# Performance work log

Measured on AMD Instinct MI355X. Metric: run time of the kernel, lower is better.

## Reference

```python
import jax, jax.numpy as jnp
import numpy as np

B, T, N, H = 256, 128, 512, 512
LB, UB = 0.0, 0.1
MAX_IT = 32  # bounded substitute for the data-dependent while loop (converges in a few iters)


def setup_inputs() -> dict:
    key = jax.random.key(0)
    ks = jax.random.split(key, 11)
    s = 1.0 / np.sqrt(H)
    u = lambda k, shape: jax.random.uniform(k, shape, jnp.float32, -s, s)
    return {
        "x": jax.random.normal(ks[0], (B, T, N), jnp.float32),
        "W_ih0": u(ks[1], (3 * H, N)), "W_hh0": u(ks[2], (3 * H, H)),
        "b_ih0": u(ks[3], (3 * H,)), "b_hh0": u(ks[4], (3 * H,)),
        "W_ih1": u(ks[5], (3 * H, H)), "W_hh1": u(ks[6], (3 * H, H)),
        "b_ih1": u(ks[7], (3 * H,)), "b_hh1": u(ks[8], (3 * H,)),
        "fc_w": u(ks[9], (N, H)), "fc_b": u(ks[10], (N,)),
    }


def gru_layer(x, W_ih, W_hh, b_ih, b_hh):
    # x: [B, T, I] -> hidden sequence [B, T, H]; matches torch.nn.GRU gate math.
    xi = jnp.einsum('bti,gi->btg', x, W_ih) + b_ih  # precompute input proj [B,T,3H]

    def step(h, xi_t):
        gh = h @ W_hh.T + b_hh
        xr, xz, xn = jnp.split(xi_t, 3, axis=-1)
        hr, hz, hn = jnp.split(gh, 3, axis=-1)
        r = jax.nn.sigmoid(xr + hr)
        z = jax.nn.sigmoid(xz + hz)
        n = jnp.tanh(xn + r * hn)
        h2 = (1.0 - z) * n + z * h
        return h2, h2

    h0 = jnp.zeros((x.shape[0], H), x.dtype)
    _, hs = jax.lax.scan(step, h0, jnp.swapaxes(xi, 0, 1))
    return jnp.swapaxes(hs, 0, 1)


def rebalance(w):
    # Water-filling: clamp to [LB, UB], redistribute clipped mass to non-capped
    # names proportionally, repeat until no weight exceeds UB. Bounded iteration
    # count with masked no-op updates (do-while semantics: body runs at least once).
    wc0 = jnp.clip(w, LB, UB)

    def body(st, _):
        old, wc, cont = st
        leftover = jnp.sum(old - wc)
        mask = wc != UB
        noms = jnp.where(mask, wc, 0.0)
        gift = leftover * noms / jnp.sum(noms)
        wc2 = wc + gift                      # gift is 0 where mask is False
        again = jnp.any(wc2 > UB)
        wc_next = jnp.where(again, jnp.clip(wc2, LB, UB), wc2)
        old_n = jnp.where(cont, wc2, old)
        wc_n = jnp.where(cont, wc_next, wc)
        return (old_n, wc_n, jnp.logical_and(cont, again)), None

    (old, wc, _), _ = jax.lax.scan(body, (w, wc0, jnp.array(True)), None, length=MAX_IT)
    return wc


def reference(x, W_ih0, W_hh0, b_ih0, b_hh0, W_ih1, W_hh1, b_ih1, b_hh1, fc_w, fc_b):
    h = gru_layer(x, W_ih0, W_hh0, b_ih0, b_hh0)
    h = gru_layer(h, W_ih1, W_hh1, b_ih1, b_hh1)
    h_t = h[:, -1, :]                        # last timestep [B, H]
    logit = h_t @ fc_w.T + fc_b              # dropout is identity in eval
    logit = jax.nn.softmax(jax.nn.silu(logit), axis=-1)
    return jax.vmap(rebalance)(logit)
```

## Files before the change

### kernel.cpp

```cpp
#include <hip/hip_runtime.h>
#include <math.h>

#define BB 256
#define TT 128
#define NN 512
#define HH 512
#define G3 1536
#define SLAB (HH * BB)
#define XSLAB (G3 * BB)
#define CH 16

typedef __attribute__((ext_vector_type(8))) short bf16x8;
typedef __attribute__((ext_vector_type(4))) float f32x4;
typedef unsigned short ushort;

__device__ __forceinline__ ushort bf16_rne(float f) {
    union { float f; unsigned u; } v; v.f = f;
    unsigned r = (v.u + 0x7fffu + ((v.u >> 16) & 1u)) >> 16;
    return (ushort)r;
}
__device__ __forceinline__ float bf16_tof(ushort h) {
    union { float f; unsigned u; } v; v.u = ((unsigned)h) << 16;
    return v.f;
}
__device__ __forceinline__ float sigm(float v) { return 1.f / (1.f + expf(-v)); }

__global__ __launch_bounds__(256) void zero6(
    float* h0s, float* h1s, ushort* H0hs, ushort* H0ls, ushort* H1hs, ushort* H1ls) {
    int i = blockIdx.x * 256 + threadIdx.x;
    int sel = i / 65536, r = i % 65536;
    if (sel == 0)      ((float2*)h0s)[r] = {0.f, 0.f};
    else if (sel == 1) ((float2*)h1s)[r] = {0.f, 0.f};
    else if (sel == 2) { if (r < 32768) ((uint2*)H0hs)[r] = {0u, 0u}; }
    else if (sel == 3) { if (r < 32768) ((uint2*)H0ls)[r] = {0u, 0u}; }
    else if (sel == 4) { if (r < 32768) ((uint2*)H1hs)[r] = {0u, 0u}; }
    else               { if (r < 32768) ((uint2*)H1ls)[r] = {0u, 0u}; }
}

__global__ __launch_bounds__(256) void convert_split(
    const float* __restrict__ in, ushort* __restrict__ hi,
    ushort* __restrict__ lo, int n) {
    int i = (blockIdx.x * 256 + threadIdx.x) * 4;
    if (i >= n) return;
    float4 v = *(const float4*)(in + i);
    float f[4] = {v.x, v.y, v.z, v.w};
    ushort h[4], l[4];
#pragma unroll
    for (int q = 0; q < 4; ++q) {
        ushort hh = bf16_rne(f[q]);
        h[q] = hh;
        l[q] = bf16_rne(f[q] - bf16_tof(hh));
    }
    *(ushort4*)(hi + i) = *(ushort4*)h;
    *(ushort4*)(lo + i) = *(ushort4*)l;
}

__global__ __launch_bounds__(64) void pack_swz(
    const float* __restrict__ Whh0, const float* __restrict__ Wih1,
    const float* __restrict__ Whh1, ushort* __restrict__ pk) {
    const int bi = blockIdx.x;
    const int it = bi & 3, kq = (bi >> 2) & 3, p = (bi >> 4) & 31, sec = bi >> 9;
    const float* W = (sec == 0) ? Whh0 : (sec == 1) ? Wih1 : Whh1;
    const int lane = threadIdx.x;
    const int l15 = lane & 15, l4 = lane >> 4;
    ushort* base = pk + (size_t)bi * 3072 + lane * 8;
#pragma unroll
    for (int g = 0; g < 3; ++g) {
        int grow = g * 512 + p * 16 + l15;
        const float* src = W + (size_t)grow * 512 + kq * 128 + it * 32 + l4 * 8;
        ushort hs[8], ls[8];
#pragma unroll
        for (int e = 0; e < 8; ++e) {
            float v = src[e];
            ushort h = bf16_rne(v);
            hs[e] = h;
            ls[e] = bf16_rne(v - bf16_tof(h));
        }
        *(uint4*)(base + g * 1024) = *(uint4*)hs;
        *(uint4*)(base + g * 1024 + 512) = *(uint4*)ls;
    }
}

__global__ __launch_bounds__(256) void xi_mfma_x(
    const ushort* __restrict__ Wh, const ushort* __restrict__ Wl,
    const float* __restrict__ x, int t0,
    const float* __restrict__ bias, float* __restrict__ out) {
    __shared__ ushort As[2][128][40];
    __shared__ ushort Bs[2][128][40];
    const int tid = threadIdx.x;
    const int n0 = blockIdx.x * 128;
    const int g0 = blockIdx.y * 128;
    const int tl = n0 >> 8, b0 = n0 & 255;
    const int tg = t0 + tl;
    const int w = tid >> 6, lane = tid & 63;
    const int wg = (w >> 1) * 64, wb = (w & 1) * 64;
    const int l15 = lane & 15, l4 = lane >> 4;
    const int sr = tid >> 2, sc = (tid & 3) * 8;

    f32x4 acc[4][4] = {};
    for (int kc = 0; kc < 512; kc += 32) {
        uint4 a0 = *(const uint4*)(Wh + (size_t)(g0 + sr) * 512 + kc + sc);
        uint4 a1 = *(const uint4*)(Wh + (size_t)(g0 + 64 + sr) * 512 + kc + sc);
        uint4 a2 = *(const uint4*)(Wl + (size_t)(g0 + sr) * 512 + kc + sc);
        uint4 a3 = *(const uint4*)(Wl + (size_t)(g0 + 64 + sr) * 512 + kc + sc);
        const float* xr0 = x + ((size_t)(b0 + sr) * TT + tg) * NN + kc + sc;
        const float* xr1 = x + ((size_t)(b0 + 64 + sr) * TT + tg) * NN + kc + sc;
        float4 f00 = *(const float4*)xr0, f01 = *(const float4*)(xr0 + 4);
        float4 f10 = *(const float4*)xr1, f11 = *(const float4*)(xr1 + 4);
        float fa[8] = {f00.x, f00.y, f00.z, f00.w, f01.x, f01.y, f01.z, f01.w};
        float fb[8] = {f10.x, f10.y, f10.z, f10.w, f11.x, f11.y, f11.z, f11.w};
        ushort h0v[8], l0v[8], h1v[8], l1v[8];
#pragma unroll
        for (int q = 0; q < 8; ++q) {
            ushort hh = bf16_rne(fa[q]);
            h0v[q] = hh; l0v[q] = bf16_rne(fa[q] - bf16_tof(hh));
            hh = bf16_rne(fb[q]);
            h1v[q] = hh; l1v[q] = bf16_rne(fb[q] - bf16_tof(hh));
        }
        __syncthreads();
        *(uint4*)&As[0][sr][sc] = a0;      *(uint4*)&As[0][64 + sr][sc] = a1;
        *(uint4*)&As[1][sr][sc] = a2;      *(uint4*)&As[1][64 + sr][sc] = a3;
        *(uint4*)&Bs[0][sr][sc] = *(uint4*)h0v;  *(uint4*)&Bs[0][64 + sr][sc] = *(uint4*)h1v;
        *(uint4*)&Bs[1][sr][sc] = *(uint4*)l0v;  *(uint4*)&Bs[1][64 + sr][sc] = *(uint4*)l1v;
        __syncthreads();
        bf16x8 ah[4], al[4], bh[4], bl[4];
#pragma unroll
        for (int i = 0; i < 4; ++i) {
            ah[i] = *(const bf16x8*)&As[0][wg + 16 * i + l15][l4 * 8];
            al[i] = *(const bf16x8*)&As[1][wg + 16 * i + l15][l4 * 8];
            bh[i] = *(const bf16x8*)&Bs[0][wb + 16 * i + l15][l4 * 8];
            bl[i] = *(const bf16x8*)&Bs[1][wb + 16 * i + l15][l4 * 8];
        }
#pragma unroll
        for (int i = 0; i < 4; ++i)
#pragma unroll
            for (int j = 0; j < 4; ++j) {
                acc[i][j] = __builtin_amdgcn_mfma_f32_16x16x32_bf16(ah[i], bh[j], acc[i][j], 0, 0, 0);
                acc[i][j] = __builtin_amdgcn_mfma_f32_16x16x32_bf16(ah[i], bl[j], acc[i][j], 0, 0, 0);
                acc[i][j] = __builtin_amdgcn_mfma_f32_16x16x32_bf16(al[i], bh[j], acc[i][j], 0, 0, 0);
            }
    }
    float* op = out + (size_t)tl * XSLAB;
#pragma unroll
    for (int i = 0; i < 4; ++i) {
        int gbase = g0 + wg + 16 * i + l4 * 4;
#pragma unroll
        for (int r = 0; r < 4; ++r) {
            float bv = bias[gbase + r];
#pragma unroll
            for (int j = 0; j < 4; ++j)
                op[(size_t)(gbase + r) * 256 + b0 + wb + 16 * j + l15] = acc[i][j][r] + bv;
        }
    }
}

template <int NG>
__device__ __forceinline__ void kreduceN(float* scr, int kq, int ct, int l15, int l4,
                                         f32x4* acc) {
    const int SS = NG * 272;
    const int slot = (kq >> 1) * 2 + ct;
    const int pos0 = (l4 * 4) * 17 + l15;
    __syncthreads();
    if (kq & 1) {
#pragma unroll
        for (int g = 0; g < NG; ++g)
#pragma unroll
            for (int q = 0; q < 4; ++q)
                scr[slot * SS + g * 272 + pos0 + q * 17] = acc[g][q];
    }
    __syncthreads();
    if (!(kq & 1)) {
#pragma unroll
        for (int g = 0; g < NG; ++g)
#pragma unroll
            for (int q = 0; q < 4; ++q)
                acc[g][q] += scr[slot * SS + g * 272 + pos0 + q * 17];
    }
    if (kq == 2) {
#pragma unroll
        for (int g = 0; g < NG; ++g)
#pragma unroll
            for (int q = 0; q < 4; ++q)
                scr[(2 + ct) * SS + g * 272 + pos0 + q * 17] = acc[g][q];
    }
    __syncthreads();
    if (kq == 0) {
#pragma unroll
        for (int g = 0; g < NG; ++g)
#pragma unroll
            for (int q = 0; q < 4; ++q)
                acc[g][q] += scr[(2 + ct) * SS + g * 272 + pos0 + q * 17];
    }
}

__global__ __launch_bounds__(512) void step_v11(
    int s, const ushort* __restrict__ pk,
    const float* __restrict__ xi0,
    const float* __restrict__ bih1,
    const float* __restrict__ bhh0, const float* __restrict__ bhh1,
    float* __restrict__ h0f, float* __restrict__ h1f,
    ushort* __restrict__ H0h, ushort* __restrict__ H0l,
    ushort* __restrict__ H1h, ushort* __restrict__ H1l) {
    __shared__ float scr[6528];
    const int bi = blockIdx.x;
    const int sec = bi >> 8, local = bi & 255;
    const int t = (sec == 0) ? s : s - 1;
    if (t < 0 || t > 127) return;
    const int p = (local & 7) * 4 + ((local >> 3) & 3);
    const int b0 = (local >> 5) * 32;
    const int tid = threadIdx.x, w = tid >> 6, lane = tid & 63;
    const int l15 = lane & 15, l4 = lane >> 4;
    const int kq = w >> 1, ct = w & 1;
    const int brow = b0 + ct * 16 + l15;

    if (sec == 0) {
        const int sl = (t - 1) & 1;
        const ushort* Bh = H0h + (size_t)sl * SLAB;
        const ushort* Bl = H0l + (size_t)sl * SLAB;
        const ushort* baseA = pk + (size_t)((0 * 32 + p) * 4 + kq) * 12288 + lane * 8;
        const ushort* bhp = Bh + (size_t)brow * 512 + kq * 128 + l4 * 8;
        const ushort* blp = Bl + (size_t)brow * 512 + kq * 128 + l4 * 8;
        f32x4 acc[3] = {};
#pragma unroll
        for (int it = 0; it < 4; ++it) {
            bf16x8 bh = *(const bf16x8*)(bhp + it * 32);
            bf16x8 bl = *(const bf16x8*)(blp + it * 32);
#pragma unroll
            for (int g = 0; g < 3; ++g) {
                const ushort* rec = baseA + (it * 3 + g) * 1024;
                bf16x8 ah = *(const bf16x8*)rec;
                bf16x8 al = *(const bf16x8*)(rec + 512);
                acc[g] = __builtin_amdgcn_mfma_f32_16x16x32_bf16(ah, bh, acc[g], 0, 0, 0);
                acc[g] = __builtin_amdgcn_mfma_f32_16x16x32_bf16(ah, bl, acc[g], 0, 0, 0);
                acc[g] = __builtin_amdgcn_mfma_f32_16x16x32_bf16(al, bh, acc[g], 0, 0, 0);
            }
        }
        kreduceN<3>(scr, kq, ct, l15, l4, acc);
        if (kq == 0) {
            const float* xi = xi0 + (size_t)(t & (CH - 1)) * XSLAB;
            const float* hpv = h0f + (size_t)((t - 1) & 1) * SLAB;
            float* hnew = h0f + (size_t)(t & 1) * SLAB;
            ushort* Hh = H0h + (size_t)(t & 1) * SLAB;
            ushort* Hl = H0l + (size_t)(t & 1) * SLAB;
            const int b = brow;
            ushort hq[4], lq[4];
#pragma unroll
            for (int q = 0; q < 4; ++q) {
                int jrow = p * 16 + l4 * 4 + q;
                float xr = xi[(size_t)jrow * 256 + b];
                float xz = xi[(size_t)(512 + jrow) * 256 + b];
                float xn = xi[(size_t)(1024 + jrow) * 256 + b];
                float hp = hpv[(size_t)jrow * 256 + b];
                float rr = sigm(xr + acc[0][q] + bhh0[jrow]);
                float zz = sigm(xz + acc[1][q] + bhh0[512 + jrow]);
                float nn = tanhf(xn + rr * (acc[2][q] + bhh0[1024 + jrow]));
                float hv = (1.f - zz) * nn + zz * hp;
                hnew[(size_t)jrow * 256 + b] = hv;
                ushort hh = bf16_rne(hv);
                hq[q] = hh;
                lq[q] = bf16_rne(hv - bf16_tof(hh));
            }
            size_t o = (size_t)b * 512 + p * 16 + l4 * 4;
            *(ushort4*)(Hh + o) = *(ushort4*)hq;
            *(ushort4*)(Hl + o) = *(ushort4*)lq;
        }
    } else {
        const int slX = t & 1, slG = (t - 1) & 1;
        const ushort* BhX = H0h + (size_t)slX * SLAB;
        const ushort* BlX = H0l + (size_t)slX * SLAB;
        const ushort* BhG = H1h + (size_t)slG * SLAB;
        const ushort* BlG = H1l + (size_t)slG * SLAB;
        const ushort* baseAX = pk + (size_t)((1 * 32 + p) * 4 + kq) * 12288 + lane * 8;
        const ushort* baseAG = pk + (size_t)((2 * 32 + p) * 4 + kq) * 12288 + lane * 8;
        const ushort* bhpX = BhX + (size_t)brow * 512 + kq * 128 + l4 * 8;
        const ushort* blpX = BlX + (size_t)brow * 512 + kq * 128 + l4 * 8;
        const ushort* bhpG = BhG + (size_t)brow * 512 + kq * 128 + l4 * 8;
        const ushort* blpG = BlG + (size_t)brow * 512 + kq * 128 + l4 * 8;
        f32x4 acc[6] = {};
#pragma unroll
        for (int it = 0; it < 4; ++it) {
            bf16x8 bhX = *(const bf16x8*)(bhpX + it * 32);
            bf16x8 blX = *(const bf16x8*)(blpX + it * 32);
            bf16x8 bhG = *(const bf16x8*)(bhpG + it * 32);
            bf16x8 blG = *(const bf16x8*)(blpG + it * 32);
#pragma unroll
            for (int g = 0; g < 3; ++g) {
                const ushort* recX = baseAX + (it * 3 + g) * 1024;
                const ushort* recG = baseAG + (it * 3 + g) * 1024;
                bf16x8 ahX = *(const bf16x8*)recX;
                bf16x8 alX = *(const bf16x8*)(recX + 512);
                bf16x8 ahG = *(const bf16x8*)recG;
                bf16x8 alG = *(const bf16x8*)(recG + 512);
                acc[g] = __builtin_amdgcn_mfma_f32_16x16x32_bf16(ahX, bhX, acc[g], 0, 0, 0);
                acc[g] = __builtin_amdgcn_mfma_f32_16x16x32_bf16(ahX, blX, acc[g], 0, 0, 0);
                acc[g] = __builtin_amdgcn_mfma_f32_16x16x32_bf16(alX, bhX, acc[g], 0, 0, 0);
                acc[3 + g] = __builtin_amdgcn_mfma_f32_16x16x32_bf16(ahG, bhG, acc[3 + g], 0, 0, 0);
                acc[3 + g] = __builtin_amdgcn_mfma_f32_16x16x32_bf16(ahG, blG, acc[3 + g], 0, 0, 0);
                acc[3 + g] = __builtin_amdgcn_mfma_f32_16x16x32_bf16(alG, bhG, acc[3 + g], 0, 0, 0);
            }
        }
        kreduceN<6>(scr, kq, ct, l15, l4, acc);
        if (kq == 0) {
            const float* hpv = h1f + (size_t)((t - 1) & 1) * SLAB;
            float* hnew = h1f + (size_t)(t & 1) * SLAB;
            ushort* Hh = H1h + (size_t)(t & 1) * SLAB;
            ushort* Hl = H1l + (size_t)(t & 1) * SLAB;
            const int b = brow;
            ushort hq[4], lq[4];
#pragma unroll
            for (int q = 0; q < 4; ++q) {
                int jrow = p * 16 + l4 * 4 + q;
                float xr = acc[0][q] + bih1[jrow];
                float xz = acc[1][q] + bih1[512 + jrow];
                float xn = acc[2][q] + bih1[1024 + jrow];
                float hp = hpv[(size_t)jrow * 256 + b];
                float rr = sigm(xr + acc[3][q] + bhh1[jrow]);
                float zz = sigm(xz + acc[4][q] + bhh1[512 + jrow]);
                float nn = tanhf(xn + rr * (acc[5][q] + bhh1[1024 + jrow]));
                float hv = (1.f - zz) * nn + zz * hp;
                hnew[(size_t)jrow * 256 + b] = hv;
                ushort hh = bf16_rne(hv);
                hq[q] = hh;
                lq[q] = bf16_rne(hv - bf16_tof(hh));
            }
            size_t o = (size_t)b * 512 + p * 16 + l4 * 4;
            *(ushort4*)(Hh + o) = *(ushort4*)hq;
            *(ushort4*)(Hl + o) = *(ushort4*)lq;
        }
    }
}


__global__ __launch_bounds__(256) void hT_to_h(
    const float* __restrict__ hT, float* __restrict__ h) {
    __shared__ float tb[64][65];
    const int tid = threadIdx.x;
    const int k0 = blockIdx.x * 64, b0 = blockIdx.y * 64;
#pragma unroll
    for (int i = 0; i < 4; ++i) {
        int r = (tid >> 4) + 16 * i, c = (tid & 15) * 4;
        float4 v = *(const float4*)(hT + (size_t)(k0 + r) * 256 + b0 + c);
        tb[c + 0][r] = v.x; tb[c + 1][r] = v.y; tb[c + 2][r] = v.z; tb[c + 3][r] = v.w;
    }
    __syncthreads();
#pragma unroll
    for (int i = 0; i < 4; ++i) {
        int r = (tid >> 4) + 16 * i, c = (tid & 15) * 4;
        float4 v;
        v.x = tb[r][c]; v.y = tb[r][c + 1]; v.z = tb[r][c + 2]; v.w = tb[r][c + 3];
        *(float4*)(h + (size_t)(b0 + r) * 512 + k0 + c) = v;
    }
}

__device__ __forceinline__ float blockReduceSum(float v, float* tmp) {
    __syncthreads();
#pragma unroll
    for (int o = 32; o; o >>= 1) v += __shfl_down(v, o);
    if ((threadIdx.x & 63) == 0) tmp[threadIdx.x >> 6] = v;
    __syncthreads();
    if (threadIdx.x == 0) tmp[4] = tmp[0] + tmp[1] + tmp[2] + tmp[3];
    __syncthreads();
    return tmp[4];
}

__device__ __forceinline__ float blockReduceMax(float v, float* tmp) {
    __syncthreads();
#pragma unroll
    for (int o = 32; o; o >>= 1) v = fmaxf(v, __shfl_down(v, o));
    if ((threadIdx.x & 63) == 0) tmp[threadIdx.x >> 6] = v;
    __syncthreads();
    if (threadIdx.x == 0) tmp[4] = fmaxf(fmaxf(tmp[0], tmp[1]), fmaxf(tmp[2], tmp[3]));
    __syncthreads();
    return tmp[4];
}

__global__ __launch_bounds__(256) void head_kernel(
    const float* __restrict__ h1, const float* __restrict__ fcw,
    const float* __restrict__ fcb, float* __restrict__ out) {
    __shared__ __align__(16) float hrow[512];
    __shared__ float wv[512];
    __shared__ float ov[512];
    __shared__ float tmp[8];
    const int b = blockIdx.x, tid = threadIdx.x;
    hrow[tid]       = h1[(size_t)b * 512 + tid];
    hrow[tid + 256] = h1[(size_t)b * 512 + 256 + tid];
    __syncthreads();

    float s[2];
#pragma unroll
    for (int q = 0; q < 2; ++q) {
        int n = tid + q * 256;
        const float* wr = fcw + (size_t)n * 512;
        float acc = 0.f;
        for (int k = 0; k < 512; k += 4) {
            float4 wq = *(const float4*)(wr + k);
            acc += wq.x * hrow[k] + wq.y * hrow[k + 1] + wq.z * hrow[k + 2] + wq.w * hrow[k + 3];
        }
        float l = acc + fcb[n];
        s[q] = l / (1.f + expf(-l));
    }

    float mx = blockReduceMax(fmaxf(s[0], s[1]), tmp);
    float e0 = expf(s[0] - mx), e1 = expf(s[1] - mx);
    float sum = blockReduceSum(e0 + e1, tmp);
    float w0 = e0 / sum, w1 = e1 / sum;

    ov[tid] = w0;       ov[tid + 256] = w1;
    wv[tid]       = fminf(fmaxf(w0, 0.f), 0.1f);
    wv[tid + 256] = fminf(fmaxf(w1, 0.f), 0.1f);
    __syncthreads();

    for (int it = 0; it < 32; ++it) {
        float wc0 = wv[tid], wc1 = wv[tid + 256];
        float o0 = ov[tid], o1 = ov[tid + 256];
        float leftover = blockReduceSum((o0 - wc0) + (o1 - wc1), tmp);
        float n0 = (wc0 != 0.1f) ? wc0 : 0.f;
        float n1 = (wc1 != 0.1f) ? wc1 : 0.f;
        float denom = blockReduceSum(n0 + n1, tmp);
        float w20 = wc0 + leftover * n0 / denom;
        float w21 = wc1 + leftover * n1 / denom;
        float fl = ((w20 > 0.1f) || (w21 > 0.1f)) ? 1.f : 0.f;
        bool again = blockReduceSum(fl, tmp) > 0.f;
        __syncthreads();
        ov[tid] = w20; ov[tid + 256] = w21;
        wv[tid]       = again ? fminf(fmaxf(w20, 0.f), 0.1f) : w20;
        wv[tid + 256] = again ? fminf(fmaxf(w21, 0.f), 0.1f) : w21;
        __syncthreads();
        if (!again) break;
    }

    out[(size_t)b * 512 + tid]       = wv[tid];
    out[(size_t)b * 512 + 256 + tid] = wv[tid + 256];
}

extern "C" void kernel_launch(void* const* d_in, const int* in_sizes, int n_in,
                              void* d_out, int out_size, void* d_ws, size_t ws_size,
                              hipStream_t stream) {
    const float* x    = (const float*)d_in[0];
    const float* Wih0 = (const float*)d_in[1];
    const float* Whh0 = (const float*)d_in[2];
    const float* bih0 = (const float*)d_in[3];
    const float* bhh0 = (const float*)d_in[4];
    const float* Wih1 = (const float*)d_in[5];
    const float* Whh1 = (const float*)d_in[6];
    const float* bih1 = (const float*)d_in[7];
    const float* bhh1 = (const float*)d_in[8];
    const float* fcw  = (const float*)d_in[9];
    const float* fcb  = (const float*)d_in[10];
    float* out = (float*)d_out;

    const size_t WHALF = (size_t)G3 * HH;
    ushort* W0h = (ushort*)d_ws;
    ushort* W0l = W0h + WHALF;
    ushort* pk  = W0l + WHALF;
    float* xi0 = (float*)(pk + (size_t)1536 * 3072);
    float* h0f = xi0 + (size_t)CH * XSLAB;
    float* h1f = h0f + 2 * (size_t)SLAB;
    float* h1n = h1f + 2 * (size_t)SLAB;
    ushort* H0h = (ushort*)(h1n + SLAB);
    ushort* H0l = H0h + 2 * (size_t)SLAB;
    ushort* H1h = H0l + 2 * (size_t)SLAB;
    ushort* H1l = H1h + 2 * (size_t)SLAB;

    convert_split<<<(G3 * HH) / 1024, 256, 0, stream>>>(Wih0, W0h, W0l, G3 * HH);
    pack_swz<<<1536, 64, 0, stream>>>(Whh0, Wih1, Whh1, pk);
    zero6<<<1536, 256, 0, stream>>>(h0f + SLAB, h1f + SLAB,
                                    H0h + SLAB, H0l + SLAB, H1h + SLAB, H1l + SLAB);

    for (int c = 0; c < TT / CH; ++c) {
        xi_mfma_x<<<dim3(CH * 2, 12), 256, 0, stream>>>(W0h, W0l, x, c * CH, bih0, xi0);
        for (int tl = 0; tl < CH; ++tl) {
            int s = c * CH + tl;
            step_v11<<<512, 512, 0, stream>>>(s, pk, xi0, bih1, bhh0, bhh1,
                                              h0f, h1f, H0h, H0l, H1h, H1l);
        }
    }
    step_v11<<<512, 512, 0, stream>>>(128, pk, xi0, bih1, bhh0, bhh1,
                                      h0f, h1f, H0h, H0l, H1h, H1l);

    hT_to_h<<<dim3(8, 4), 256, 0, stream>>>(h1f + SLAB, h1n);
    head_kernel<<<BB, 256, 0, stream>>>(h1n, fcw, fcb, out);
}
```

Before: 2.196 ms.

## Fuse input projection into recurrent step kernel and drop fp32 hidden state

The layer-0 input projection now runs as a third section of the per-timestep step kernel, computing timestep s+8 alongside the recurrence, so the separate chunked xi launches go away and that work overlaps the latency-bound recurrent steps. The fp32 hidden-state buffers are removed; the previous hidden value is rebuilt from its bf16 hi/lo split, which saves global writes and removes the transpose kernel before the head. The costs are 768 blocks per step instead of 512, extra register and LDS pressure, a ring-buffer dependency on the 8-step lookahead fitting in the 16-slot xi buffer, and a slight precision loss from reconstructing h out of two bf16 halves.

New measurement: 2.653 ms. +20.8%, slower.

```diff
diff --git a/kernel.cpp b/kernel.cpp
--- a/kernel.cpp
+++ b/kernel.cpp
@@ -25,16 +25,26 @@
 }
 __device__ __forceinline__ float sigm(float v) { return 1.f / (1.f + expf(-v)); }
 
-__global__ __launch_bounds__(256) void zero6(
-    float* h0s, float* h1s, ushort* H0hs, ushort* H0ls, ushort* H1hs, ushort* H1ls) {
+__device__ __forceinline__ void split8(float4 a, float4 b, uint4& hi, uint4& lo) {
+    float f[8] = {a.x, a.y, a.z, a.w, b.x, b.y, b.z, b.w};
+    ushort hs[8], ls[8];
+#pragma unroll
+    for (int q = 0; q < 8; ++q) {
+        ushort h = bf16_rne(f[q]);
+        hs[q] = h;
+        ls[q] = bf16_rne(f[q] - bf16_tof(h));
+    }
+    hi = *(uint4*)hs;
+    lo = *(uint4*)ls;
+}
+
+__global__ __launch_bounds__(256) void zero4(
+    ushort* a, ushort* b, ushort* c, ushort* d) {
     int i = blockIdx.x * 256 + threadIdx.x;
-    int sel = i / 65536, r = i % 65536;
-    if (sel == 0)      ((float2*)h0s)[r] = {0.f, 0.f};
-    else if (sel == 1) ((float2*)h1s)[r] = {0.f, 0.f};
-    else if (sel == 2) { if (r < 32768) ((uint2*)H0hs)[r] = {0u, 0u}; }
-    else if (sel == 3) { if (r < 32768) ((uint2*)H0ls)[r] = {0u, 0u}; }
-    else if (sel == 4) { if (r < 32768) ((uint2*)H1hs)[r] = {0u, 0u}; }
-    else               { if (r < 32768) ((uint2*)H1ls)[r] = {0u, 0u}; }
+    int sel = i >> 14, r = i & 16383;
+    uint4 z = {0u, 0u, 0u, 0u};
+    ushort* p = (sel == 0) ? a : (sel == 1) ? b : (sel == 2) ? c : d;
+    ((uint4*)p)[r] = z;
 }
 
 __global__ __launch_bounds__(256) void convert_split(
@@ -107,21 +117,14 @@
         const float* xr1 = x + ((size_t)(b0 + 64 + sr) * TT + tg) * NN + kc + sc;
         float4 f00 = *(const float4*)xr0, f01 = *(const float4*)(xr0 + 4);
         float4 f10 = *(const float4*)xr1, f11 = *(const float4*)(xr1 + 4);
-        float fa[8] = {f00.x, f00.y, f00.z, f00.w, f01.x, f01.y, f01.z, f01.w};
-        float fb[8] = {f10.x, f10.y, f10.z, f10.w, f11.x, f11.y, f11.z, f11.w};
-        ushort h0v[8], l0v[8], h1v[8], l1v[8];
-#pragma unroll
-        for (int q = 0; q < 8; ++q) {
-            ushort hh = bf16_rne(fa[q]);
-            h0v[q] = hh; l0v[q] = bf16_rne(fa[q] - bf16_tof(hh));
-            hh = bf16_rne(fb[q]);
-            h1v[q] = hh; l1v[q] = bf16_rne(fb[q] - bf16_tof(hh));
-        }
+        uint4 h0v, l0v, h1v, l1v;
+        split8(f00, f01, h0v, l0v);
+        split8(f10, f11, h1v, l1v);
         __syncthreads();
         *(uint4*)&As[0][sr][sc] = a0;      *(uint4*)&As[0][64 + sr][sc] = a1;
         *(uint4*)&As[1][sr][sc] = a2;      *(uint4*)&As[1][64 + sr][sc] = a3;
-        *(uint4*)&Bs[0][sr][sc] = *(uint4*)h0v;  *(uint4*)&Bs[0][64 + sr][sc] = *(uint4*)h1v;
-        *(uint4*)&Bs[1][sr][sc] = *(uint4*)l0v;  *(uint4*)&Bs[1][64 + sr][sc] = *(uint4*)l1v;
+        *(uint4*)&Bs[0][sr][sc] = h0v;     *(uint4*)&Bs[0][64 + sr][sc] = h1v;
+        *(uint4*)&Bs[1][sr][sc] = l0v;     *(uint4*)&Bs[1][64 + sr][sc] = l1v;
         __syncthreads();
         bf16x8 ah[4], al[4], bh[4], bl[4];
 #pragma unroll
@@ -193,19 +196,18 @@
     }
 }
 
-__global__ __launch_bounds__(512) void step_v11(
+__global__ __launch_bounds__(512) void step_v12(
     int s, const ushort* __restrict__ pk,
-    const float* __restrict__ xi0,
-    const float* __restrict__ bih1,
+    const float* __restrict__ x,
+    const ushort* __restrict__ W0h, const ushort* __restrict__ W0l,
+    float* __restrict__ xi0,
+    const float* __restrict__ bih0, const float* __restrict__ bih1,
     const float* __restrict__ bhh0, const float* __restrict__ bhh1,
-    float* __restrict__ h0f, float* __restrict__ h1f,
     ushort* __restrict__ H0h, ushort* __restrict__ H0l,
     ushort* __restrict__ H1h, ushort* __restrict__ H1l) {
     __shared__ float scr[6528];
     const int bi = blockIdx.x;
     const int sec = bi >> 8, local = bi & 255;
-    const int t = (sec == 0) ? s : s - 1;
-    if (t < 0 || t > 127) return;
     const int p = (local & 7) * 4 + ((local >> 3) & 3);
     const int b0 = (local >> 5) * 32;
     const int tid = threadIdx.x, w = tid >> 6, lane = tid & 63;
@@ -214,6 +216,8 @@
     const int brow = b0 + ct * 16 + l15;
 
     if (sec == 0) {
+        const int t = s;
+        if (t > 127) return;
         const int sl = (t - 1) & 1;
         const ushort* Bh = H0h + (size_t)sl * SLAB;
         const ushort* Bl = H0l + (size_t)sl * SLAB;
@@ -238,11 +242,16 @@
         kreduceN<3>(scr, kq, ct, l15, l4, acc);
         if (kq == 0) {
             const float* xi = xi0 + (size_t)(t & (CH - 1)) * XSLAB;
-            const float* hpv = h0f + (size_t)((t - 1) & 1) * SLAB;
-            float* hnew = h0f + (size_t)(t & 1) * SLAB;
+            const ushort* Hph = H0h + (size_t)sl * SLAB;
+            const ushort* Hpl = H0l + (size_t)sl * SLAB;
             ushort* Hh = H0h + (size_t)(t & 1) * SLAB;
             ushort* Hl = H0l + (size_t)(t & 1) * SLAB;
             const int b = brow;
+            size_t o = (size_t)b * 512 + p * 16 + l4 * 4;
+            ushort4 hph = *(const ushort4*)(Hph + o);
+            ushort4 hpl = *(const ushort4*)(Hpl + o);
+            const ushort* hph_ = (const ushort*)&hph;
+            const ushort* hpl_ = (const ushort*)&hpl;
             ushort hq[4], lq[4];
 #pragma unroll
             for (int q = 0; q < 4; ++q) {
@@ -250,21 +259,21 @@
                 float xr = xi[(size_t)jrow * 256 + b];
                 float xz = xi[(size_t)(512 + jrow) * 256 + b];
                 float xn = xi[(size_t)(1024 + jrow) * 256 + b];
-                float hp = hpv[(size_t)jrow * 256 + b];
+                float hp = bf16_tof(hph_[q]) + bf16_tof(hpl_[q]);
                 float rr = sigm(xr + acc[0][q] + bhh0[jrow]);
                 float zz = sigm(xz + acc[1][q] + bhh0[512 + jrow]);
                 float nn = tanhf(xn + rr * (acc[2][q] + bhh0[1024 + jrow]));
                 float hv = (1.f - zz) * nn + zz * hp;
-                hnew[(size_t)jrow * 256 + b] = hv;
                 ushort hh = bf16_rne(hv);
                 hq[q] = hh;
                 lq[q] = bf16_rne(hv - bf16_tof(hh));
             }
-            size_t o = (size_t)b * 512 + p * 16 + l4 * 4;
             *(ushort4*)(Hh + o) = *(ushort4*)hq;
             *(ushort4*)(Hl + o) = *(ushort4*)lq;
         }
-    } else {
+    } else if (sec == 1) {
+        const int t = s - 1;
+        if (t < 0 || t > 127) return;
         const int slX = t & 1, slG = (t - 1) & 1;
         const ushort* BhX = H0h + (size_t)slX * SLAB;
         const ushort* BlX = H0l + (size_t)slX * SLAB;
@@ -301,11 +310,17 @@
         }
         kreduceN<6>(scr, kq, ct, l15, l4, acc);
         if (kq == 0) {
-            const float* hpv = h1f + (size_t)((t - 1) & 1) * SLAB;
-            float* hnew = h1f + (size_t)(t & 1) * SLAB;
+            const int slp = (t - 1) & 1;
+            const ushort* Hph = H1h + (size_t)slp * SLAB;
+            const ushort* Hpl = H1l + (size_t)slp * SLAB;
             ushort* Hh = H1h + (size_t)(t & 1) * SLAB;
             ushort* Hl = H1l + (size_t)(t & 1) * SLAB;
             const int b = brow;
+            size_t o = (size_t)b * 512 + p * 16 + l4 * 4;
+            ushort4 hph = *(const ushort4*)(Hph + o);
+            ushort4 hpl = *(const ushort4*)(Hpl + o);
+            const ushort* hph_ = (const ushort*)&hph;
+            const ushort* hpl_ = (const ushort*)&hpl;
             ushort hq[4], lq[4];
 #pragma unroll
             for (int q = 0; q < 4; ++q) {
@@ -313,44 +328,56 @@
                 float xr = acc[0][q] + bih1[jrow];
                 float xz = acc[1][q] + bih1[512 + jrow];
                 float xn = acc[2][q] + bih1[1024 + jrow];
-                float hp = hpv[(size_t)jrow * 256 + b];
+                float hp = bf16_tof(hph_[q]) + bf16_tof(hpl_[q]);
                 float rr = sigm(xr + acc[3][q] + bhh1[jrow]);
                 float zz = sigm(xz + acc[4][q] + bhh1[512 + jrow]);
                 float nn = tanhf(xn + rr * (acc[5][q] + bhh1[1024 + jrow]));
                 float hv = (1.f - zz) * nn + zz * hp;
-                hnew[(size_t)jrow * 256 + b] = hv;
                 ushort hh = bf16_rne(hv);
                 hq[q] = hh;
                 lq[q] = bf16_rne(hv - bf16_tof(hh));
             }
-            size_t o = (size_t)b * 512 + p * 16 + l4 * 4;
             *(ushort4*)(Hh + o) = *(ushort4*)hq;
             *(ushort4*)(Hl + o) = *(ushort4*)lq;
         }
-    }
-}
-
-
-__global__ __launch_bounds__(256) void hT_to_h(
-    const float* __restrict__ hT, float* __restrict__ h) {
-    __shared__ float tb[64][65];
-    const int tid = threadIdx.x;
-    const int k0 = blockIdx.x * 64, b0 = blockIdx.y * 64;
-#pragma unroll
-    for (int i = 0; i < 4; ++i) {
-        int r = (tid >> 4) + 16 * i, c = (tid & 15) * 4;
-        float4 v = *(const float4*)(hT + (size_t)(k0 + r) * 256 + b0 + c);
-        tb[c + 0][r] = v.x; tb[c + 1][r] = v.y; tb[c + 2][r] = v.z; tb[c + 3][r] = v.w;
-    }
-    __syncthreads();
-#pragma unroll
-    for (int i = 0; i < 4; ++i) {
-        int r = (tid >> 4) + 16 * i, c = (tid & 15) * 4;
-        float4 v;
-        v.x = tb[r][c]; v.y = tb[r][c + 1]; v.z = tb[r][c + 2]; v.w = tb[r][c + 3];
-        *(float4*)(h + (size_t)(b0 + r) * 512 + k0 + c) = v;
-    }
-}
+    } else {
+        const int tt = s + 8;
+        if (tt > 127) return;
+        const float* xb = x + ((size_t)brow * TT + tt) * NN;
+        f32x4 acc[3] = {};
+#pragma unroll
+        for (int it = 0; it < 4; ++it) {
+            const int k = kq * 128 + it * 32 + l4 * 8;
+            float4 f0 = *(const float4*)(xb + k);
+            float4 f1 = *(const float4*)(xb + k + 4);
+            uint4 bhv, blv;
+            split8(f0, f1, bhv, blv);
+            bf16x8 bh = *(bf16x8*)&bhv, bl = *(bf16x8*)&blv;
+#pragma unroll
+            for (int g = 0; g < 3; ++g) {
+                int grow = g * 512 + p * 16 + l15;
+                bf16x8 ah = *(const bf16x8*)(W0h + (size_t)grow * 512 + k);
+                bf16x8 al = *(const bf16x8*)(W0l + (size_t)grow * 512 + k);
+                acc[g] = __builtin_amdgcn_mfma_f32_16x16x32_bf16(ah, bh, acc[g], 0, 0, 0);
+                acc[g] = __builtin_amdgcn_mfma_f32_16x16x32_bf16(ah, bl, acc[g], 0, 0, 0);
+                acc[g] = __builtin_amdgcn_mfma_f32_16x16x32_bf16(al, bh, acc[g], 0, 0, 0);
+            }
+        }
+        kreduceN<3>(scr, kq, ct, l15, l4, acc);
+        if (kq == 0) {
+            float* xo = xi0 + (size_t)(tt & (CH - 1)) * XSLAB;
+            const int b = brow;
+#pragma unroll
+            for (int g = 0; g < 3; ++g)
+#pragma unroll
+                for (int q = 0; q < 4; ++q) {
+                    int grow = g * 512 + p * 16 + l4 * 4 + q;
+                    xo[(size_t)grow * 256 + b] = acc[g][q] + bih0[grow];
+                }
+        }
+    }
+}
+
 
 __device__ __forceinline__ float blockReduceSum(float v, float* tmp) {
     __syncthreads();
@@ -375,15 +402,19 @@
 }
 
 __global__ __launch_bounds__(256) void head_kernel(
-    const float* __restrict__ h1, const float* __restrict__ fcw,
-    const float* __restrict__ fcb, float* __restrict__ out) {
+    const ushort* __restrict__ H1hs, const ushort* __restrict__ H1ls,
+    const float* __restrict__ fcw, const float* __restrict__ fcb,
+    float* __restrict__ out) {
     __shared__ __align__(16) float hrow[512];
     __shared__ float wv[512];
     __shared__ float ov[512];
     __shared__ float tmp[8];
     const int b = blockIdx.x, tid = threadIdx.x;
-    hrow[tid]       = h1[(size_t)b * 512 + tid];
-    hrow[tid + 256] = h1[(size_t)b * 512 + 256 + tid];
+    {
+        size_t o = (size_t)b * 512 + tid;
+        hrow[tid]       = bf16_tof(H1hs[o]) + bf16_tof(H1ls[o]);
+        hrow[tid + 256] = bf16_tof(H1hs[o + 256]) + bf16_tof(H1ls[o + 256]);
+    }
     __syncthreads();
 
     float s[2];
@@ -454,30 +485,20 @@
     ushort* W0l = W0h + WHALF;
     ushort* pk  = W0l + WHALF;
     float* xi0 = (float*)(pk + (size_t)1536 * 3072);
-    float* h0f = xi0 + (size_t)CH * XSLAB;
-    float* h1f = h0f + 2 * (size_t)SLAB;
-    float* h1n = h1f + 2 * (size_t)SLAB;
-    ushort* H0h = (ushort*)(h1n + SLAB);
+    ushort* H0h = (ushort*)(xi0 + (size_t)CH * XSLAB);
     ushort* H0l = H0h + 2 * (size_t)SLAB;
     ushort* H1h = H0l + 2 * (size_t)SLAB;
     ushort* H1l = H1h + 2 * (size_t)SLAB;
 
     convert_split<<<(G3 * HH) / 1024, 256, 0, stream>>>(Wih0, W0h, W0l, G3 * HH);
     pack_swz<<<1536, 64, 0, stream>>>(Whh0, Wih1, Whh1, pk);
-    zero6<<<1536, 256, 0, stream>>>(h0f + SLAB, h1f + SLAB,
-                                    H0h + SLAB, H0l + SLAB, H1h + SLAB, H1l + SLAB);
-
-    for (int c = 0; c < TT / CH; ++c) {
-        xi_mfma_x<<<dim3(CH * 2, 12), 256, 0, stream>>>(W0h, W0l, x, c * CH, bih0, xi0);
-        for (int tl = 0; tl < CH; ++tl) {
-            int s = c * CH + tl;
-            step_v11<<<512, 512, 0, stream>>>(s, pk, xi0, bih1, bhh0, bhh1,
-                                              h0f, h1f, H0h, H0l, H1h, H1l);
-        }
-    }
-    step_v11<<<512, 512, 0, stream>>>(128, pk, xi0, bih1, bhh0, bhh1,
-                                      h0f, h1f, H0h, H0l, H1h, H1l);
-
-    hT_to_h<<<dim3(8, 4), 256, 0, stream>>>(h1f + SLAB, h1n);
-    head_kernel<<<BB, 256, 0, stream>>>(h1n, fcw, fcb, out);
-}
+    zero4<<<256, 256, 0, stream>>>(H0h + SLAB, H0l + SLAB, H1h + SLAB, H1l + SLAB);
+    xi_mfma_x<<<dim3(16, 12), 256, 0, stream>>>(W0h, W0l, x, 0, bih0, xi0);
+
+    for (int s = 0; s <= 128; ++s)
+        step_v12<<<768, 512, 0, stream>>>(s, pk, x, W0h, W0l, xi0,
+                                          bih0, bih1, bhh0, bhh1,
+                                          H0h, H0l, H1h, H1l);
+
+    head_kernel<<<BB, 256, 0, stream>>>(H1h + SLAB, H1l + SLAB, fcw, fcb, out);
+}
```
